# Kernel tuning notes

Measured on AMD Instinct MI355X. Metric: run time of the kernel, lower is better.

Reference implementation:

```python
import jax, jax.numpy as jnp
import numpy as np


def setup_inputs() -> dict:
    key = jax.random.key(0)
    ks = jax.random.split(key, 9)
    B, T, C = 4, 2048, 2048
    E, I, SI = 8, 1408, 5632
    s = lambda k, shape, fan_in: jax.random.normal(k, shape, jnp.float32) * (fan_in ** -0.5)
    return {
        "x": jax.random.normal(ks[0], (B, T, C), jnp.float32),
        "gate_w": s(ks[1], (C, E), C),                  # router: x @ gate_w -> [N,E]
        "expert_gate_w": s(ks[2], (E, C, I), C),        # stacked gate_proj weights
        "expert_up_w": s(ks[3], (E, C, I), C),          # stacked up_proj weights
        "expert_down_w": s(ks[4], (E, I, C), I),        # stacked down_proj weights
        "shared_gate_w": s(ks[5], (C, SI), C),
        "shared_up_w": s(ks[6], (C, SI), C),
        "shared_down_w": s(ks[7], (SI, C), SI),
        "shared_expert_gate_w": s(ks[8], (C, 1), C),
        "top_k": 4,
    }


def reference(x, gate_w, expert_gate_w, expert_up_w, expert_down_w,
              shared_gate_w, shared_up_w, shared_down_w, shared_expert_gate_w, top_k):
    B, T, C = x.shape
    E = gate_w.shape[1]
    xf = x.reshape(-1, C)                      # [N, C]
    N = xf.shape[0]

    # --- router: softmax (fp32) -> top-k -> renormalize ---
    logits = xf @ gate_w                       # [N, E]
    probs = jax.nn.softmax(logits.astype(jnp.float32), axis=-1)
    w, idx = jax.lax.top_k(probs, top_k)       # [N, k]
    w = w / jnp.sum(w, axis=-1, keepdims=True)

    # dense combine gates [N, E]: zero for non-selected experts (equivalent to
    # the torch dispatch/sort/combine: each token gets weight w_k on expert idx_k)
    gates = jnp.zeros((N, E), jnp.float32).at[jnp.arange(N)[:, None], idx].add(w)

    # --- per-expert SwiGLU MLP, accumulated via scan over experts ---
    def step(acc, ew):
        wg, wu, wd, g = ew                     # wg/wu: [C,I], wd: [I,C], g: [N]
        h = jax.nn.silu(xf @ wg) * (xf @ wu)   # [N, I]
        return acc + g[:, None] * (h @ wd), None

    routed, _ = jax.lax.scan(
        step, jnp.zeros_like(xf),
        (expert_gate_w, expert_up_w, expert_down_w, gates.T))

    # --- shared expert with sigmoid gate ---
    shared = (jax.nn.silu(xf @ shared_gate_w) * (xf @ shared_up_w)) @ shared_down_w
    sg = jax.nn.sigmoid(xf @ shared_expert_gate_w)   # [N, 1]

    return (routed + sg * shared).reshape(B, T, C)
```

## Files before the change

kernel.cpp:

```cpp
#include <hip/hip_runtime.h>
#include <hip/hip_bf16.h>
#include <stdint.h>


typedef float f32x4 __attribute__((ext_vector_type(4)));
typedef int   i32x4 __attribute__((ext_vector_type(4)));
typedef __hip_bfloat16 bf16;

#define DEV __device__ __forceinline__

DEV void mfma16(f32x4& c, const i32x4& a, const i32x4& b) {
    asm("v_mfma_f32_16x16x32_bf16 %0, %1, %2, %0" : "+v"(c) : "v"(a), "v"(b));
}

template<int ROWS>
DEV void stage(const bf16* gtile, long ldK, char* lds, int tid) {
    const int wid = tid >> 6, lane = tid & 63;
    const int swz = ((lane & 7) ^ (lane >> 3)) << 4;
    constexpr int NISS = (ROWS * 128) / 4096;
    #pragma unroll
    for (int i = 0; i < NISS; i++) {
        const int o = i * 4096 + wid * 1024;
        const int row = (o >> 7) + (lane >> 3);
        const char* ga = (const char*)gtile + (long)row * (ldK * 2) + swz;
        __builtin_amdgcn_global_load_lds(
            (const __attribute__((address_space(1))) void*)ga,
            (__attribute__((address_space(3))) void*)(lds + o), 16, 0, 0);
    }
}

template<int ROWS>
DEV void stage_idx(const char* base, const long* roff, int ktb, char* lds,
                   int tid, int swz) {
    const int wid = tid >> 6;
    constexpr int NISS = (ROWS * 128) / 4096;
    #pragma unroll
    for (int i = 0; i < NISS; i++) {
        const int o = i * 4096 + wid * 1024;
        const char* ga = base + roff[i] + ktb + swz;
        __builtin_amdgcn_global_load_lds(
            (const __attribute__((address_space(1))) void*)ga,
            (__attribute__((address_space(3))) void*)(lds + o), 16, 0, 0);
    }
}

DEV i32x4 ldsfrag(const char* lds, int row, int kbyte) {
    const int off = (row << 7) + (kbyte ^ ((row & 7) << 4));
    return *(const i32x4*)(lds + off);
}

DEV void tcore(unsigned short (*t)[72], const float* __restrict__ src,
               bf16* __restrict__ dst, long Cd, long dld, int cb, int rb,
               int tid) {
    const int s = tid & 15, g = tid >> 4;
    #pragma unroll
    for (int i = 0; i < 4; i++) {
        const int r = i * 16 + g;
        const float4 v = *(const float4*)(src + (long)(rb + r) * Cd + cb + 4 * s);
        union { bf16 h[4]; ushort4 u; } cu;
        cu.h[0] = __float2bfloat16(v.x); cu.h[1] = __float2bfloat16(v.y);
        cu.h[2] = __float2bfloat16(v.z); cu.h[3] = __float2bfloat16(v.w);
        *(ushort4*)&t[r][4 * s] = cu.u;
    }
    __syncthreads();
    #pragma unroll
    for (int i = 0; i < 4; i++) {
        const int c = i * 16 + g;
        ushort4 u;
        u.x = t[4 * s + 0][c]; u.y = t[4 * s + 1][c];
        u.z = t[4 * s + 2][c]; u.w = t[4 * s + 3][c];
        *(ushort4*)((unsigned short*)dst + (long)(cb + c) * dld + rb + 4 * s) = u;
    }
}

__global__ __launch_bounds__(256) void convt_gu(const float* __restrict__ egw,
        const float* __restrict__ euw, const float* __restrict__ sgw,
        const float* __restrict__ suw, bf16* __restrict__ Wea,
        bf16* __restrict__ Web, bf16* __restrict__ Wsa, bf16* __restrict__ Wsb) {
    __shared__ unsigned short t[64][72];
    const int z = blockIdx.z, cb = blockIdx.x * 64, rb = blockIdx.y * 64;
    const float* src; bf16* dst; long Cd;
    if (z < 8)       { src = egw + (long)z * 2048 * 1408;        dst = Wea + (long)z * 1408 * 2048;        Cd = 1408; }
    else if (z < 16) { src = euw + (long)(z - 8) * 2048 * 1408;  dst = Web + (long)(z - 8) * 1408 * 2048;  Cd = 1408; }
    else if (z < 20) { src = sgw + (long)(z - 16) * 1408;        dst = Wsa + (long)(z - 16) * 1408 * 2048; Cd = 5632; }
    else             { src = suw + (long)(z - 20) * 1408;        dst = Wsb + (long)(z - 20) * 1408 * 2048; Cd = 5632; }
    tcore(t, src, dst, Cd, 2048, cb, rb, threadIdx.x);
}

__global__ __launch_bounds__(256) void convt_dn(const float* __restrict__ sdw,
        const float* __restrict__ edw, bf16* __restrict__ Wsd,
        bf16* __restrict__ Wed) {
    __shared__ unsigned short t[64][72];
    const int z = blockIdx.z, cb = blockIdx.x * 64, rb = blockIdx.y * 64;
    if (z < 4)
        tcore(t, sdw + (long)z * 1408 * 2048, Wsd + (long)z * 1408,
              2048, 5632, cb, rb, threadIdx.x);
    else
        tcore(t, edw + (long)(z - 4) * 1408 * 2048, Wed + (long)(z - 4) * 2048 * 1408,
              2048, 1408, cb, rb, threadIdx.x);
}

__global__ __launch_bounds__(256) void convt_dns(const float* __restrict__ sdw,
        bf16* __restrict__ Wsd) {
    __shared__ unsigned short t[64][72];
    const int z = blockIdx.z, cb = blockIdx.x * 64, rb = blockIdx.y * 64;
    tcore(t, sdw + (long)z * 1408 * 2048, Wsd + (long)z * 1408,
          2048, 5632, cb, rb, threadIdx.x);
}
__global__ __launch_bounds__(256) void convt_dne(const float* __restrict__ edw,
        bf16* __restrict__ Wed) {
    __shared__ unsigned short t[64][72];
    const int z = blockIdx.z, cb = blockIdx.x * 64, rb = blockIdx.y * 64;
    tcore(t, edw + (long)z * 1408 * 2048, Wed + (long)z * 2048 * 1408,
          2048, 1408, cb, rb, threadIdx.x);
}

__global__ __launch_bounds__(256) void tcvt(const float* __restrict__ srcA,
        bf16* __restrict__ dstA, const float* __restrict__ srcB,
        bf16* __restrict__ dstB, int Cd, long dld, long sz, long dz,
        int zsplit) {
    __shared__ float t[64][65];
    long z = blockIdx.z;
    const float* src; bf16* dst;
    if ((int)z < zsplit) { src = srcA; dst = dstA; }
    else { src = srcB; dst = dstB; z -= zsplit; }
    src += z * sz; dst += z * dz;
    const int cb = blockIdx.x * 64, rb = blockIdx.y * 64;
    const int tx = threadIdx.x & 63, ty = threadIdx.x >> 6;
    #pragma unroll
    for (int i = 0; i < 16; i++) {
        const int r = ty + i * 4;
        t[r][tx] = src[(long)(rb + r) * Cd + cb + tx];
    }
    __syncthreads();
    #pragma unroll
    for (int i = 0; i < 16; i++) {
        const int c = ty + i * 4;
        dst[(long)(cb + c) * dld + rb + tx] = __float2bfloat16(t[tx][c]);
    }
}

__global__ __launch_bounds__(256) void cvtrt(const float* __restrict__ x,
        const float* __restrict__ gw, const float* __restrict__ segw,
        bf16* __restrict__ xb, int* __restrict__ tidx, float* __restrict__ tw,
        float* __restrict__ sg) {
    const int lane = threadIdx.x & 63;
    const long t = (long)blockIdx.x * 4 + (threadIdx.x >> 6);
    const float4* xr = (const float4*)(x + t * 2048);
    ushort4* xo = (ushort4*)(xb + t * 2048);
    float a[9];
    #pragma unroll
    for (int e = 0; e < 9; e++) a[e] = 0.f;
    #pragma unroll
    for (int i = 0; i < 8; i++) {
        const int c4 = i * 64 + lane;
        const float4 v = xr[c4];
        union { bf16 h[4]; ushort4 u; } cu;
        cu.h[0] = __float2bfloat16(v.x); cu.h[1] = __float2bfloat16(v.y);
        cu.h[2] = __float2bfloat16(v.z); cu.h[3] = __float2bfloat16(v.w);
        xo[c4] = cu.u;
        const int c = c4 * 4;
        const float xv[4] = { v.x, v.y, v.z, v.w };
        #pragma unroll
        for (int j = 0; j < 4; j++) {
            const float4* g4 = (const float4*)(gw + (long)(c + j) * 8);
            const float4 g0 = g4[0], g1 = g4[1];
            a[0] += xv[j] * g0.x; a[1] += xv[j] * g0.y;
            a[2] += xv[j] * g0.z; a[3] += xv[j] * g0.w;
            a[4] += xv[j] * g1.x; a[5] += xv[j] * g1.y;
            a[6] += xv[j] * g1.z; a[7] += xv[j] * g1.w;
            a[8] += xv[j] * segw[c + j];
        }
    }
    #pragma unroll
    for (int e = 0; e < 9; e++) {
        #pragma unroll
        for (int o = 32; o; o >>= 1) a[e] += __shfl_xor(a[e], o, 64);
    }
    if (lane == 0) {
        float m = a[0];
        #pragma unroll
        for (int e = 1; e < 8; e++) m = fmaxf(m, a[e]);
        float p[8]; float s = 0.f;
        #pragma unroll
        for (int e = 0; e < 8; e++) { p[e] = expf(a[e] - m); s += p[e]; }
        #pragma unroll
        for (int e = 0; e < 8; e++) p[e] /= s;
        bool used[8] = {false,false,false,false,false,false,false,false};
        float wsum = 0.f; int idx[4]; float wv[4];
        for (int k = 0; k < 4; k++) {
            float best = -1.f; int bi = 0;
            for (int e = 0; e < 8; e++)
                if (!used[e] && p[e] > best) { best = p[e]; bi = e; }
            used[bi] = true; idx[k] = bi; wv[k] = best; wsum += best;
        }
        int4 iv; float4 wv4;
        iv.x = idx[0]; iv.y = idx[1]; iv.z = idx[2]; iv.w = idx[3];
        wv4.x = wv[0] / wsum; wv4.y = wv[1] / wsum;
        wv4.z = wv[2] / wsum; wv4.w = wv[3] / wsum;
        ((int4*)tidx)[t] = iv;
        ((float4*)tw)[t] = wv4;
        sg[t] = 1.f / (1.f + expf(-a[8]));
    }
}

__global__ __launch_bounds__(256) void build_lists(const int* __restrict__ tidx,
        const float* __restrict__ tw, int* __restrict__ tok,
        float* __restrict__ wl, int* __restrict__ cnt, int* __restrict__ inv,
        int N) {
    const int e = blockIdx.x;
    const int tid = threadIdx.x;
    const int per = N / 256;
    __shared__ int csum[256];
    int c = 0;
    for (int i = 0; i < per; i++) {
        const int4 id4 = ((const int4*)tidx)[tid * per + i];
        if (id4.x == e || id4.y == e || id4.z == e || id4.w == e) c++;
    }
    csum[tid] = c;
    __syncthreads();
    for (int o = 1; o < 256; o <<= 1) {
        const int v = (tid >= o) ? csum[tid - o] : 0;
        __syncthreads();
        csum[tid] += v;
        __syncthreads();
    }
    int pos = csum[tid] - c;
    if (tid == 255) cnt[e] = csum[255];
    for (int i = 0; i < per; i++) {
        const int t = tid * per + i;
        const int4   id4 = ((const int4*)tidx)[t];
        const float4 w4  = ((const float4*)tw)[t];
        float w = 0.f; int hit = 0; int k = 0;
        if      (id4.x == e) { w = w4.x; hit = 1; k = 0; }
        else if (id4.y == e) { w = w4.y; hit = 1; k = 1; }
        else if (id4.z == e) { w = w4.z; hit = 1; k = 2; }
        else if (id4.w == e) { w = w4.w; hit = 1; k = 3; }
        if (hit) {
            tok[(long)e * N + pos] = t;
            wl[(long)e * N + pos] = w;
            inv[t * 4 + k] = pos;
            pos++;
        }
    }
}

__global__ void scan8(const int* __restrict__ cnt, int* __restrict__ starts) {
    if (threadIdx.x == 0) {
        int s = 0;
        for (int e = 0; e < 8; e++) { starts[e] = s; s += cnt[e]; }
        starts[8] = s;
    }
}

__global__ __launch_bounds__(256) void megadual(const bf16* __restrict__ A0,
        const int* __restrict__ tok, const int* __restrict__ cnt,
        const int* __restrict__ starts, int nExpZ, int e0,
        const bf16* __restrict__ Wea, const bf16* __restrict__ Web, long ebz,
        const bf16* __restrict__ Wsa, const bf16* __restrict__ Wsb,
        bf16* __restrict__ He, bf16* __restrict__ Hs,
        const float* __restrict__ wl, const float* __restrict__ sg, int K) {
    __shared__ __align__(128) char Al[16384];
    __shared__ __align__(128) char Gl[8192];
    __shared__ __align__(128) char Ul[8192];
    const int z = blockIdx.z;
    const bf16 *BG, *BU; bf16* H; long hld, n0; const float* sc;
    const int* ridx; int Me;
    if (z < nExpZ) {
        const int e = e0 + z;
        Me = cnt[e];
        ridx = tok + (long)e * 8192;
        BG = Wea + (long)z * ebz; BU = Web + (long)z * ebz;
        H = He + ((long)starts[e] - starts[e0]) * 1408;
        hld = 1408; sc = wl + (long)e * 8192;
        n0 = (long)blockIdx.y * 64;
    } else {
        Me = 8192; ridx = nullptr;
        BG = Wsa; BU = Wsb; H = Hs; hld = 5632; sc = sg;
        n0 = (long)((z - nExpZ) * gridDim.y + blockIdx.y) * 64;
    }
    const long m0 = (long)blockIdx.x * 128;
    if (m0 >= Me) return;
    const int tid = threadIdx.x, lane = tid & 63, wid = tid >> 6;
    const int wm = (wid >> 1) * 64, wn = (wid & 1) * 32;
    const int l15 = lane & 15, lhi = lane >> 4;
    const int swz = ((lane & 7) ^ (lane >> 3)) << 4;
    long roffA[4];
    #pragma unroll
    for (int i = 0; i < 4; i++) {
        const int rit = ((i * 4096 + wid * 1024) >> 7) + (lane >> 3);
        int g = (int)m0 + rit;
        if (ridx) g = ridx[g < Me ? g : Me - 1];
        roffA[i] = (long)g * (K * 2);
    }
    f32x4 ag[4][2] = {}; f32x4 au[4][2] = {};
    for (int kt = 0; kt < K; kt += 64) {
        stage_idx<128>((const char*)A0, roffA, kt * 2, Al, tid, swz);
        stage<64>(BG + n0 * K + kt, (long)K, Gl, tid);
        stage<64>(BU + n0 * K + kt, (long)K, Ul, tid);
        __syncthreads();
        #pragma unroll
        for (int ks = 0; ks < 2; ks++) {
            const int kb = ks * 64 + lhi * 16;
            i32x4 af[4], bg[2], bu[2];
            #pragma unroll
            for (int mi = 0; mi < 4; mi++) af[mi] = ldsfrag(Al, wm + mi * 16 + l15, kb);
            #pragma unroll
            for (int ni = 0; ni < 2; ni++) {
                bg[ni] = ldsfrag(Gl, wn + ni * 16 + l15, kb);
                bu[ni] = ldsfrag(Ul, wn + ni * 16 + l15, kb);
            }
            #pragma unroll
            for (int mi = 0; mi < 4; mi++) {
                #pragma unroll
                for (int ni = 0; ni < 2; ni++) {
                    mfma16(ag[mi][ni], af[mi], bg[ni]);
                    mfma16(au[mi][ni], af[mi], bu[ni]);
                }
            }
        }
        __syncthreads();
    }
    asm volatile("s_nop 7\n\ts_nop 7\n\ts_nop 7");
    #pragma unroll
    for (int mi = 0; mi < 4; mi++) {
        #pragma unroll
        for (int r = 0; r < 4; r++) {
            const int pos = (int)m0 + wm + mi * 16 + lhi * 4 + r;
            if (pos < Me) {
                const float s = sc[pos];
                #pragma unroll
                for (int ni = 0; ni < 2; ni++) {
                    const float gv = ag[mi][ni][r], uv = au[mi][ni][r];
                    const float h = (gv / (1.f + expf(-gv))) * uv * s;
                    H[(long)pos * hld + n0 + wn + ni * 16 + l15] = __float2bfloat16(h);
                }
            }
        }
    }
}

template<int TAG>
__global__ __launch_bounds__(256) void gemm_down_t(const bf16* __restrict__ A,
        const bf16* __restrict__ BT, float* __restrict__ C,
        const int* __restrict__ ridx, const int* __restrict__ cntp, int Mfix,
        const int* __restrict__ starts, int ia, int ib,
        int K, long ldc, int beta) {
    __shared__ __align__(128) char Al[16384];
    __shared__ __align__(128) char Bl[16384];
    const int Me = cntp ? *cntp : Mfix;
    const long m0 = (long)blockIdx.y * 128;
    if (m0 >= Me) return;
    if (starts) A += ((long)starts[ia] - starts[ib]) * K;
    const int tid = threadIdx.x, lane = tid & 63, wid = tid >> 6;
    const long n0 = (long)blockIdx.x * 128;
    const int wm = (wid >> 1) * 64, wn = (wid & 1) * 64;
    const int l15 = lane & 15, lhi = lane >> 4;
    f32x4 acc[4][4] = {};
    for (int kt = 0; kt < K; kt += 64) {
        stage<128>(A  + m0 * K + kt, (long)K, Al, tid);
        stage<128>(BT + n0 * K + kt, (long)K, Bl, tid);
        __syncthreads();
        #pragma unroll
        for (int ks = 0; ks < 2; ks++) {
            const int kb = ks * 64 + lhi * 16;
            i32x4 af[4], bfr[4];
            #pragma unroll
            for (int mi = 0; mi < 4; mi++) af[mi]  = ldsfrag(Al, wm + mi * 16 + l15, kb);
            #pragma unroll
            for (int ni = 0; ni < 4; ni++) bfr[ni] = ldsfrag(Bl, wn + ni * 16 + l15, kb);
            #pragma unroll
            for (int mi = 0; mi < 4; mi++) {
                #pragma unroll
                for (int ni = 0; ni < 4; ni++) mfma16(acc[mi][ni], af[mi], bfr[ni]);
            }
        }
        __syncthreads();
    }
    asm volatile("s_nop 7\n\ts_nop 7\n\ts_nop 7");
    #pragma unroll
    for (int mi = 0; mi < 4; mi++) {
        #pragma unroll
        for (int r = 0; r < 4; r++) {
            const int pos = (int)m0 + wm + mi * 16 + lhi * 4 + r;
            if (pos < Me) {
                const long orow = ridx ? (long)ridx[pos] : (long)pos;
                #pragma unroll
                for (int ni = 0; ni < 4; ni++) {
                    const long ci = orow * ldc + n0 + wn + ni * 16 + l15;
                    float v = acc[mi][ni][r];
                    if (beta) v += C[ci];
                    C[ci] = v;
                }
            }
        }
    }
}

__global__ __launch_bounds__(256) void downfuse(const bf16* __restrict__ Hs,
        const bf16* __restrict__ Wsd, const bf16* __restrict__ De,
        const int* __restrict__ tidx, const int* __restrict__ inv,
        const int* __restrict__ starts, float* __restrict__ out, int K) {
    __shared__ __align__(128) char Al[16384];
    __shared__ __align__(128) char Bl[16384];
    __shared__ int sst[8];
    const int tid = threadIdx.x, lane = tid & 63, wid = tid >> 6;
    if (tid < 8) sst[tid] = starts[tid];
    const long m0 = (long)blockIdx.y * 128;
    const long n0 = (long)blockIdx.x * 128;
    const int wm = (wid >> 1) * 64, wn = (wid & 1) * 64;
    const int l15 = lane & 15, lhi = lane >> 4;
    f32x4 acc[4][4] = {};
    for (int kt = 0; kt < K; kt += 64) {
        stage<128>(Hs + m0 * K + kt, (long)K, Al, tid);
        stage<128>(Wsd + n0 * K + kt, (long)K, Bl, tid);
        __syncthreads();
        #pragma unroll
        for (int ks = 0; ks < 2; ks++) {
            const int kb = ks * 64 + lhi * 16;
            i32x4 af[4], bfr[4];
            #pragma unroll
            for (int mi = 0; mi < 4; mi++) af[mi]  = ldsfrag(Al, wm + mi * 16 + l15, kb);
            #pragma unroll
            for (int ni = 0; ni < 4; ni++) bfr[ni] = ldsfrag(Bl, wn + ni * 16 + l15, kb);
            #pragma unroll
            for (int mi = 0; mi < 4; mi++) {
                #pragma unroll
                for (int ni = 0; ni < 4; ni++) mfma16(acc[mi][ni], af[mi], bfr[ni]);
            }
        }
        __syncthreads();
    }
    asm volatile("s_nop 7\n\ts_nop 7\n\ts_nop 7");
    #pragma unroll
    for (int mi = 0; mi < 4; mi++) {
        #pragma unroll
        for (int r = 0; r < 4; r++) {
            const long t = m0 + wm + mi * 16 + lhi * 4 + r;
            const int4 e4 = ((const int4*)tidx)[t];
            const int4 p4 = ((const int4*)inv)[t];
            long rr[4];
            rr[0] = (long)sst[e4.x] + p4.x; rr[1] = (long)sst[e4.y] + p4.y;
            rr[2] = (long)sst[e4.z] + p4.z; rr[3] = (long)sst[e4.w] + p4.w;
            #pragma unroll
            for (int ni = 0; ni < 4; ni++) {
                const long col = n0 + wn + ni * 16 + l15;
                float v = acc[mi][ni][r];
                #pragma unroll
                for (int k = 0; k < 4; k++)
                    v += __bfloat162float(De[rr[k] * 2048 + col]);
                out[t * 2048 + col] = v;
            }
        }
    }
}

__global__ __launch_bounds__(256) void megadown(const bf16* __restrict__ He,
        const bf16* __restrict__ Wd0, long wz, bf16* __restrict__ De,
        const int* __restrict__ cnt, const int* __restrict__ starts, int K) {
    __shared__ __align__(128) char Al[16384];
    __shared__ __align__(128) char Bl[16384];
    const int z = blockIdx.z;
    const int Me = cnt[z];
    const long m0 = (long)blockIdx.y * 128;
    if (m0 >= Me) return;
    const bf16* A  = He + (long)starts[z] * K;
    const bf16* BT = Wd0 + (long)z * wz;
    const int tid = threadIdx.x, lane = tid & 63, wid = tid >> 6;
    const long n0 = (long)blockIdx.x * 128;
    const int wm = (wid >> 1) * 64, wn = (wid & 1) * 64;
    const int l15 = lane & 15, lhi = lane >> 4;
    f32x4 acc[4][4] = {};
    for (int kt = 0; kt < K; kt += 64) {
        stage<128>(A  + m0 * K + kt, (long)K, Al, tid);
        stage<128>(BT + n0 * K + kt, (long)K, Bl, tid);
        __syncthreads();
        #pragma unroll
        for (int ks = 0; ks < 2; ks++) {
            const int kb = ks * 64 + lhi * 16;
            i32x4 af[4], bfr[4];
            #pragma unroll
            for (int mi = 0; mi < 4; mi++) af[mi]  = ldsfrag(Al, wm + mi * 16 + l15, kb);
            #pragma unroll
            for (int ni = 0; ni < 4; ni++) bfr[ni] = ldsfrag(Bl, wn + ni * 16 + l15, kb);
            #pragma unroll
            for (int mi = 0; mi < 4; mi++) {
                #pragma unroll
                for (int ni = 0; ni < 4; ni++) mfma16(acc[mi][ni], af[mi], bfr[ni]);
            }
        }
        __syncthreads();
    }
    asm volatile("s_nop 7\n\ts_nop 7\n\ts_nop 7");
    #pragma unroll
    for (int mi = 0; mi < 4; mi++) {
        #pragma unroll
        for (int r = 0; r < 4; r++) {
            const int pos = (int)m0 + wm + mi * 16 + lhi * 4 + r;
            if (pos < Me) {
                const long orow = (long)starts[z] + pos;
                #pragma unroll
                for (int ni = 0; ni < 4; ni++) {
                    De[orow * 2048 + n0 + wn + ni * 16 + l15]
                        = __float2bfloat16(acc[mi][ni][r]);
                }
            }
        }
    }
}

__global__ __launch_bounds__(256) void reduce4(const bf16* __restrict__ De,
        const int* __restrict__ tidx, const int* __restrict__ inv,
        const int* __restrict__ starts, float* __restrict__ out) {
    const long t = blockIdx.x;
    const int c = threadIdx.x * 8;
    const int4 e4 = ((const int4*)tidx)[t];
    const int4 p4 = ((const int4*)inv)[t];
    long r[4];
    r[0] = (long)starts[e4.x] + p4.x; r[1] = (long)starts[e4.y] + p4.y;
    r[2] = (long)starts[e4.z] + p4.z; r[3] = (long)starts[e4.w] + p4.w;
    float4* o = (float4*)(out + t * 2048 + c);
    float4 o0 = o[0], o1 = o[1];
    float acc[8] = { o0.x, o0.y, o0.z, o0.w, o1.x, o1.y, o1.z, o1.w };
    #pragma unroll
    for (int k = 0; k < 4; k++) {
        const uint4 v = *(const uint4*)(De + r[k] * 2048 + c);
        const unsigned w[4] = { v.x, v.y, v.z, v.w };
        #pragma unroll
        for (int j = 0; j < 4; j++) {
            union { unsigned u; float f; } lo, hi;
            lo.u = (w[j] & 0xffffu) << 16;
            hi.u = w[j] & 0xffff0000u;
            acc[j * 2]     += lo.f;
            acc[j * 2 + 1] += hi.f;
        }
    }
    o[0] = make_float4(acc[0], acc[1], acc[2], acc[3]);
    o[1] = make_float4(acc[4], acc[5], acc[6], acc[7]);
}

extern "C" void kernel_launch(void* const* d_in, const int* in_sizes, int n_in,
                              void* d_out, int out_size, void* d_ws, size_t ws_size,
                              hipStream_t stream) {
    const int N = 8192, Cdim = 2048, E = 8, I = 1408, SI = 5632;

    const float* x    = (const float*)d_in[0];
    const float* gw   = (const float*)d_in[1];
    const float* egw  = (const float*)d_in[2];
    const float* euw  = (const float*)d_in[3];
    const float* edw  = (const float*)d_in[4];
    const float* sgw  = (const float*)d_in[5];
    const float* suw  = (const float*)d_in[6];
    const float* sdw  = (const float*)d_in[7];
    const float* segw = (const float*)d_in[8];
    float* out = (float*)d_out;

    char* ws = (char*)d_ws;
    size_t off = 0;
    auto alloc = [&](size_t bytes) { char* p = ws + off; off += (bytes + 255) & ~(size_t)255; return p; };

    bf16*  xb     = (bf16*) alloc((size_t)N * Cdim * 2);
    int*   tidx   = (int*)  alloc((size_t)N * 4 * 4);
    float* tw     = (float*)alloc((size_t)N * 4 * 4);
    float* sg     = (float*)alloc((size_t)N * 4);
    int*   tok    = (int*)  alloc((size_t)E * N * 4);
    float* wl     = (float*)alloc((size_t)E * N * 4);
    int*   inv    = (int*)  alloc((size_t)N * 4 * 4);
    int*   cnt    = (int*)  alloc(256);
    int*   starts = (int*)  alloc(256);
    const size_t commonEnd = off;

    const size_t EWSLOT = (size_t)E * I * Cdim * 2;
    const size_t SWSLOT = (size_t)SI * Cdim * 2;
    const size_t HROWS  = (size_t)4 * N;
    const size_t mergedNeed = commonEnd + 2 * EWSLOT + 2 * SWSLOT
                            + (size_t)N * SI * 2 + HROWS * I * 2 + 4096;
    const size_t fusedNeed  = mergedNeed + EWSLOT;

    cvtrt<<<N / 4, 256, 0, stream>>>(x, gw, segw, xb, tidx, tw, sg);
    build_lists<<<E, 256, 0, stream>>>(tidx, tw, tok, wl, cnt, inv, N);
    scan8<<<1, 64, 0, stream>>>(cnt, starts);

    if (ws_size >= mergedNeed) {
        char* wreg = (char*)alloc(2 * EWSLOT + 2 * SWSLOT);
        bf16* Wea = (bf16*)wreg;
        bf16* Web = (bf16*)(wreg + EWSLOT);
        bf16* Wsa = (bf16*)(wreg + 2 * EWSLOT);
        bf16* Wsb = (bf16*)(wreg + 2 * EWSLOT + SWSLOT);
        bf16* Hs  = (bf16*)alloc((size_t)N * SI * 2);
        bf16* He  = (bf16*)alloc(HROWS * I * 2);
        bf16* Wsd = xb;
        bf16* De  = (bf16*)wreg;

        convt_gu<<<dim3(22, 32, 24), 256, 0, stream>>>(
                egw, euw, sgw, suw, Wea, Web, Wsa, Wsb);
        megadual<<<dim3(N / 128, I / 64, E + 4), 256, 0, stream>>>(xb,
                tok, cnt, starts, E, 0, Wea, Web, (long)I * Cdim,
                Wsa, Wsb, He, Hs, wl, sg, Cdim);

        if (ws_size >= fusedNeed) {
            bf16* Wed = (bf16*)alloc(EWSLOT);
            convt_dn<<<dim3(32, 22, 12), 256, 0, stream>>>(sdw, edw, Wsd, Wed);
            megadown<<<dim3(Cdim / 128, N / 128, E), 256, 0, stream>>>(
                    He, Wed, (long)Cdim * I, De, cnt, starts, I);
            downfuse<<<dim3(Cdim / 128, N / 128), 256, 0, stream>>>(
                    Hs, Wsd, De, tidx, inv, starts, out, SI);
        } else {
            bf16* Wed = Hs;
            convt_dns<<<dim3(32, 22, 4), 256, 0, stream>>>(sdw, Wsd);
            gemm_down_t<0><<<dim3(Cdim / 128, N / 128), 256, 0, stream>>>(
                    Hs, Wsd, out, nullptr, nullptr, N, nullptr, 0, 0,
                    SI, (long)Cdim, 0);
            convt_dne<<<dim3(32, 22, 8), 256, 0, stream>>>(edw, Wed);
            megadown<<<dim3(Cdim / 128, N / 128, E), 256, 0, stream>>>(
                    He, Wed, (long)Cdim * I, De, cnt, starts, I);
            reduce4<<<N, 256, 0, stream>>>(De, tidx, inv, starts, out);
        }
        return;
    }

    bf16* Wa = (bf16*)alloc(SWSLOT);
    bf16* Wb = (bf16*)alloc(SWSLOT);
    bf16* Wc = (bf16*)alloc(SWSLOT);
    bf16* Hs = (bf16*)alloc((size_t)N * SI * 2);
    bf16* He = (bf16*)alloc(HROWS * I * 2);
    if (off > ws_size) return;

    tcvt<<<dim3(SI / 64, Cdim / 64, 2), 256, 0, stream>>>(
            sgw, Wa, suw, Wb, SI, (long)Cdim, 0, 0, 1);
    tcvt<<<dim3(Cdim / 64, SI / 64, 1), 256, 0, stream>>>(
            sdw, Wc, nullptr, nullptr, Cdim, (long)SI, 0, 0, 1);
    megadual<<<dim3(N / 128, I / 64, 4), 256, 0, stream>>>(xb,
            tok, cnt, starts, 0, 0, nullptr, nullptr, 0,
            Wa, Wb, nullptr, Hs, wl, sg, Cdim);
    gemm_down_t<0><<<dim3(Cdim / 128, N / 128), 256, 0, stream>>>(
            Hs, Wc, out, nullptr, nullptr, N, nullptr, 0, 0, SI, (long)Cdim, 0);

    for (int b = 0; b < 2; b++) {
        const int e0 = b * 4;
        tcvt<<<dim3(I / 64, Cdim / 64, 8), 256, 0, stream>>>(
                egw + (long)e0 * Cdim * I, Wa, euw + (long)e0 * Cdim * I, Wb,
                I, (long)Cdim, (long)Cdim * I, (long)I * Cdim, 4);
        megadual<<<dim3(N / 128, I / 64, 4), 256, 0, stream>>>(xb,
                tok, cnt, starts, 4, e0, Wa, Wb, (long)I * Cdim,
                nullptr, nullptr, He, nullptr, wl, sg, Cdim);
        tcvt<<<dim3(Cdim / 64, I / 64, 4), 256, 0, stream>>>(
                edw + (long)e0 * I * Cdim, Wc, nullptr, nullptr,
                Cdim, (long)I, (long)I * Cdim, (long)Cdim * I, 4);
        for (int z = 0; z < 4; z++) {
            gemm_down_t<1><<<dim3(Cdim / 128, N / 128), 256, 0, stream>>>(
                    He, Wc + (long)z * Cdim * I, out,
                    tok + (long)(e0 + z) * N, cnt + e0 + z, 0,
                    starts, e0 + z, e0, I, (long)Cdim, 1);
        }
    }
}
```

Baseline: 1.399 ms.

## Reuse dead buffers so the fused shared-down epilogue path always runs

Drops the workspace-size check that chose between the fused down path and the unfused fallback. Expert down weights are now converted in two halves of four experts into the dead activation buffer `xb`, each followed by its own megadown launch. The shared down weights are then converted into the expert hidden buffer once it is no longer needed. This lets `downfuse`, which folds the reduction of the top-4 expert outputs into the shared-down GEMM epilogue, run without the extra workspace slot, so the separate `gemm_down_t` and `reduce4` passes are avoided. The cost is extra kernel launches and serialised conversion steps when workspace was already large enough for the old fused path.

```diff
diff --git a/kernel.cpp b/kernel.cpp
--- a/kernel.cpp
+++ b/kernel.cpp
@@ -87,19 +87,6 @@
     tcore(t, src, dst, Cd, 2048, cb, rb, threadIdx.x);
 }
 
-__global__ __launch_bounds__(256) void convt_dn(const float* __restrict__ sdw,
-        const float* __restrict__ edw, bf16* __restrict__ Wsd,
-        bf16* __restrict__ Wed) {
-    __shared__ unsigned short t[64][72];
-    const int z = blockIdx.z, cb = blockIdx.x * 64, rb = blockIdx.y * 64;
-    if (z < 4)
-        tcore(t, sdw + (long)z * 1408 * 2048, Wsd + (long)z * 1408,
-              2048, 5632, cb, rb, threadIdx.x);
-    else
-        tcore(t, edw + (long)(z - 4) * 1408 * 2048, Wed + (long)(z - 4) * 2048 * 1408,
-              2048, 1408, cb, rb, threadIdx.x);
-}
-
 __global__ __launch_bounds__(256) void convt_dns(const float* __restrict__ sdw,
         bf16* __restrict__ Wsd) {
     __shared__ unsigned short t[64][72];
@@ -107,11 +94,11 @@
     tcore(t, sdw + (long)z * 1408 * 2048, Wsd + (long)z * 1408,
           2048, 5632, cb, rb, threadIdx.x);
 }
-__global__ __launch_bounds__(256) void convt_dne(const float* __restrict__ edw,
+__global__ __launch_bounds__(256) void convt_dne(const float* __restrict__ edw0,
         bf16* __restrict__ Wed) {
     __shared__ unsigned short t[64][72];
     const int z = blockIdx.z, cb = blockIdx.x * 64, rb = blockIdx.y * 64;
-    tcore(t, edw + (long)z * 1408 * 2048, Wed + (long)z * 2048 * 1408,
+    tcore(t, edw0 + (long)z * 1408 * 2048, Wed + (long)z * 2048 * 1408,
           2048, 1408, cb, rb, threadIdx.x);
 }
 
@@ -397,64 +384,6 @@
     }
 }
 
-__global__ __launch_bounds__(256) void downfuse(const bf16* __restrict__ Hs,
-        const bf16* __restrict__ Wsd, const bf16* __restrict__ De,
-        const int* __restrict__ tidx, const int* __restrict__ inv,
-        const int* __restrict__ starts, float* __restrict__ out, int K) {
-    __shared__ __align__(128) char Al[16384];
-    __shared__ __align__(128) char Bl[16384];
-    __shared__ int sst[8];
-    const int tid = threadIdx.x, lane = tid & 63, wid = tid >> 6;
-    if (tid < 8) sst[tid] = starts[tid];
-    const long m0 = (long)blockIdx.y * 128;
-    const long n0 = (long)blockIdx.x * 128;
-    const int wm = (wid >> 1) * 64, wn = (wid & 1) * 64;
-    const int l15 = lane & 15, lhi = lane >> 4;
-    f32x4 acc[4][4] = {};
-    for (int kt = 0; kt < K; kt += 64) {
-        stage<128>(Hs + m0 * K + kt, (long)K, Al, tid);
-        stage<128>(Wsd + n0 * K + kt, (long)K, Bl, tid);
-        __syncthreads();
-        #pragma unroll
-        for (int ks = 0; ks < 2; ks++) {
-            const int kb = ks * 64 + lhi * 16;
-            i32x4 af[4], bfr[4];
-            #pragma unroll
-            for (int mi = 0; mi < 4; mi++) af[mi]  = ldsfrag(Al, wm + mi * 16 + l15, kb);
-            #pragma unroll
-            for (int ni = 0; ni < 4; ni++) bfr[ni] = ldsfrag(Bl, wn + ni * 16 + l15, kb);
-            #pragma unroll
-            for (int mi = 0; mi < 4; mi++) {
-                #pragma unroll
-                for (int ni = 0; ni < 4; ni++) mfma16(acc[mi][ni], af[mi], bfr[ni]);
-            }
-        }
-        __syncthreads();
-    }
-    asm volatile("s_nop 7\n\ts_nop 7\n\ts_nop 7");
-    #pragma unroll
-    for (int mi = 0; mi < 4; mi++) {
-        #pragma unroll
-        for (int r = 0; r < 4; r++) {
-            const long t = m0 + wm + mi * 16 + lhi * 4 + r;
-            const int4 e4 = ((const int4*)tidx)[t];
-            const int4 p4 = ((const int4*)inv)[t];
-            long rr[4];
-            rr[0] = (long)sst[e4.x] + p4.x; rr[1] = (long)sst[e4.y] + p4.y;
-            rr[2] = (long)sst[e4.z] + p4.z; rr[3] = (long)sst[e4.w] + p4.w;
-            #pragma unroll
-            for (int ni = 0; ni < 4; ni++) {
-                const long col = n0 + wn + ni * 16 + l15;
-                float v = acc[mi][ni][r];
-                #pragma unroll
-                for (int k = 0; k < 4; k++)
-                    v += __bfloat162float(De[rr[k] * 2048 + col]);
-                out[t * 2048 + col] = v;
-            }
-        }
-    }
-}
-
 __global__ __launch_bounds__(256) void megadown(const bf16* __restrict__ He,
         const bf16* __restrict__ Wd0, long wz, bf16* __restrict__ De,
         const int* __restrict__ cnt, const int* __restrict__ starts, int K) {
@@ -509,6 +438,64 @@
     }
 }
 
+__global__ __launch_bounds__(256) void downfuse(const bf16* __restrict__ Hs,
+        const bf16* __restrict__ Wsd, const bf16* __restrict__ De,
+        const int* __restrict__ tidx, const int* __restrict__ inv,
+        const int* __restrict__ starts, float* __restrict__ out, int K) {
+    __shared__ __align__(128) char Al[16384];
+    __shared__ __align__(128) char Bl[16384];
+    __shared__ int sst[8];
+    const int tid = threadIdx.x, lane = tid & 63, wid = tid >> 6;
+    if (tid < 8) sst[tid] = starts[tid];
+    const long m0 = (long)blockIdx.y * 128;
+    const long n0 = (long)blockIdx.x * 128;
+    const int wm = (wid >> 1) * 64, wn = (wid & 1) * 64;
+    const int l15 = lane & 15, lhi = lane >> 4;
+    f32x4 acc[4][4] = {};
+    for (int kt = 0; kt < K; kt += 64) {
+        stage<128>(Hs + m0 * K + kt, (long)K, Al, tid);
+        stage<128>(Wsd + n0 * K + kt, (long)K, Bl, tid);
+        __syncthreads();
+        #pragma unroll
+        for (int ks = 0; ks < 2; ks++) {
+            const int kb = ks * 64 + lhi * 16;
+            i32x4 af[4], bfr[4];
+            #pragma unroll
+            for (int mi = 0; mi < 4; mi++) af[mi]  = ldsfrag(Al, wm + mi * 16 + l15, kb);
+            #pragma unroll
+            for (int ni = 0; ni < 4; ni++) bfr[ni] = ldsfrag(Bl, wn + ni * 16 + l15, kb);
+            #pragma unroll
+            for (int mi = 0; mi < 4; mi++) {
+                #pragma unroll
+                for (int ni = 0; ni < 4; ni++) mfma16(acc[mi][ni], af[mi], bfr[ni]);
+            }
+        }
+        __syncthreads();
+    }
+    asm volatile("s_nop 7\n\ts_nop 7\n\ts_nop 7");
+    #pragma unroll
+    for (int mi = 0; mi < 4; mi++) {
+        #pragma unroll
+        for (int r = 0; r < 4; r++) {
+            const long t = m0 + wm + mi * 16 + lhi * 4 + r;
+            const int4 e4 = ((const int4*)tidx)[t];
+            const int4 p4 = ((const int4*)inv)[t];
+            long rr[4];
+            rr[0] = (long)sst[e4.x] + p4.x; rr[1] = (long)sst[e4.y] + p4.y;
+            rr[2] = (long)sst[e4.z] + p4.z; rr[3] = (long)sst[e4.w] + p4.w;
+            #pragma unroll
+            for (int ni = 0; ni < 4; ni++) {
+                const long col = n0 + wn + ni * 16 + l15;
+                float v = acc[mi][ni][r];
+                #pragma unroll
+                for (int k = 0; k < 4; k++)
+                    v += __bfloat162float(De[rr[k] * 2048 + col]);
+                out[t * 2048 + col] = v;
+            }
+        }
+    }
+}
+
 __global__ __launch_bounds__(256) void reduce4(const bf16* __restrict__ De,
         const int* __restrict__ tidx, const int* __restrict__ inv,
         const int* __restrict__ starts, float* __restrict__ out) {
@@ -575,7 +562,6 @@
     const size_t HROWS  = (size_t)4 * N;
     const size_t mergedNeed = commonEnd + 2 * EWSLOT + 2 * SWSLOT
                             + (size_t)N * SI * 2 + HROWS * I * 2 + 4096;
-    const size_t fusedNeed  = mergedNeed + EWSLOT;
 
     cvtrt<<<N / 4, 256, 0, stream>>>(x, gw, segw, xb, tidx, tw, sg);
     build_lists<<<E, 256, 0, stream>>>(tidx, tw, tok, wl, cnt, inv, N);
@@ -589,8 +575,9 @@
         bf16* Wsb = (bf16*)(wreg + 2 * EWSLOT + SWSLOT);
         bf16* Hs  = (bf16*)alloc((size_t)N * SI * 2);
         bf16* He  = (bf16*)alloc(HROWS * I * 2);
-        bf16* Wsd = xb;
-        bf16* De  = (bf16*)wreg;
+        bf16* De   = (bf16*)wreg;
+        bf16* Wedh = xb;
+        bf16* Wsd  = He;
 
         convt_gu<<<dim3(22, 32, 24), 256, 0, stream>>>(
                 egw, euw, sgw, suw, Wea, Web, Wsa, Wsb);
@@ -598,24 +585,17 @@
                 tok, cnt, starts, E, 0, Wea, Web, (long)I * Cdim,
                 Wsa, Wsb, He, Hs, wl, sg, Cdim);
 
-        if (ws_size >= fusedNeed) {
-            bf16* Wed = (bf16*)alloc(EWSLOT);
-            convt_dn<<<dim3(32, 22, 12), 256, 0, stream>>>(sdw, edw, Wsd, Wed);
-            megadown<<<dim3(Cdim / 128, N / 128, E), 256, 0, stream>>>(
-                    He, Wed, (long)Cdim * I, De, cnt, starts, I);
-            downfuse<<<dim3(Cdim / 128, N / 128), 256, 0, stream>>>(
-                    Hs, Wsd, De, tidx, inv, starts, out, SI);
-        } else {
-            bf16* Wed = Hs;
-            convt_dns<<<dim3(32, 22, 4), 256, 0, stream>>>(sdw, Wsd);
-            gemm_down_t<0><<<dim3(Cdim / 128, N / 128), 256, 0, stream>>>(
-                    Hs, Wsd, out, nullptr, nullptr, N, nullptr, 0, 0,
-                    SI, (long)Cdim, 0);
-            convt_dne<<<dim3(32, 22, 8), 256, 0, stream>>>(edw, Wed);
-            megadown<<<dim3(Cdim / 128, N / 128, E), 256, 0, stream>>>(
-                    He, Wed, (long)Cdim * I, De, cnt, starts, I);
-            reduce4<<<N, 256, 0, stream>>>(De, tidx, inv, starts, out);
-        }
+        convt_dne<<<dim3(32, 22, 4), 256, 0, stream>>>(edw, Wedh);
+        megadown<<<dim3(Cdim / 128, N / 128, 4), 256, 0, stream>>>(
+                He, Wedh, (long)Cdim * I, De, cnt, starts, I);
+        convt_dne<<<dim3(32, 22, 4), 256, 0, stream>>>(
+                edw + (long)4 * I * Cdim, Wedh);
+        megadown<<<dim3(Cdim / 128, N / 128, 4), 256, 0, stream>>>(
+                He, Wedh, (long)Cdim * I, De, cnt + 4, starts + 4, I);
+
+        convt_dns<<<dim3(32, 22, 4), 256, 0, stream>>>(sdw, Wsd);
+        downfuse<<<dim3(Cdim / 128, N / 128), 256, 0, stream>>>(
+                Hs, Wsd, De, tidx, inv, starts, out, SI);
         return;
     }
 
```

After: 1.431 ms. 1.02x slower.
